# Optimization experiments

Measured on AMD Instinct MI355X. Metric: run time of the kernel, lower is better.

## Reference

```python
import jax, jax.numpy as jnp
import numpy as np

D_K = 64
EPS = 1e-6


def setup_inputs() -> dict:
    key = jax.random.key(0)
    ks = jax.random.split(key, 6)
    B, S, D2, DV = 4, 2048, 1024, 64
    q = jax.random.normal(ks[0], (B, S, D2), dtype=jnp.float32)
    k = jax.random.normal(ks[1], (B, S, D2), dtype=jnp.float32)
    v = jax.random.normal(ks[2], (B, S, D2), dtype=jnp.float32)
    mask = jax.random.randint(ks[3], (B, S, S), 0, 2) == 1
    V = jax.random.normal(ks[4], (1, DV), dtype=jnp.float32)
    fc_w = jax.random.normal(ks[5], (D2, DV), dtype=jnp.float32) * (1.0 / np.sqrt(DV))
    fc_b = jnp.zeros((D2,), dtype=jnp.float32)
    ln_g = jnp.ones((D2,), dtype=jnp.float32)
    ln_b = jnp.zeros((D2,), dtype=jnp.float32)
    return {"q": q, "k": k, "v": v, "mask": mask, "V": V,
            "fc_w": fc_w, "fc_b": fc_b, "ln_g": ln_g, "ln_b": ln_b}


def _layer_norm(x, g, b):
    mu = jnp.mean(x, axis=-1, keepdims=True)
    var = jnp.var(x, axis=-1, keepdims=True)
    return (x - mu) * jax.lax.rsqrt(var + EPS) * g + b


def reference(q, k, v, mask, V, fc_w, fc_b, ln_g, ln_b):
    residual = q
    qn = _layer_norm(q, ln_g, ln_b)
    # scaled dot-product scores (no softmax in this variant)
    attn = jnp.einsum('bsd,btd->bst', qn / jnp.sqrt(jnp.float32(D_K)), k)
    attn = jnp.where(mask, 0.0, attn)  # masked_fill with 0
    # v_ = V broadcast over (batch, seq, key); attn @ v_ == row-sum outer V
    output = jnp.sum(attn, axis=-1, keepdims=True) * V  # [B,S,d_v]
    output = output @ fc_w.T + fc_b                     # [B,S,2*d_model]
    output = output + residual
    return (output, attn)
```

## Files before the change

kernel.cpp:

```cpp
#include <hip/hip_runtime.h>
#include <hip/hip_bf16.h>
#include <cstdint>

#define S_LEN 2048
#define D2_   1024
#define DV_   64
#define NB_   4

typedef __bf16 bf16x8 __attribute__((ext_vector_type(8)));
typedef float  f32x4  __attribute__((ext_vector_type(4)));
typedef int    i32x4  __attribute__((ext_vector_type(4)));

__device__ __forceinline__ unsigned short f2bf(float f) {
  union { float f; unsigned int u; } v; v.f = f;
  unsigned int r = v.u + 0x7fffu + ((v.u >> 16) & 1u);
  return (unsigned short)(r >> 16);
}

__device__ __forceinline__ void async16(const unsigned short* g, unsigned short* l) {
  __builtin_amdgcn_global_load_lds(
      (__attribute__((address_space(1))) void*)g,
      (__attribute__((address_space(3))) void*)l,
      16, 0, 0);
}

__global__ void __launch_bounds__(256) prep_kernel(
    const float* __restrict__ q, const float* __restrict__ k,
    const float* __restrict__ gam, const float* __restrict__ bet,
    const float* __restrict__ V, const float* __restrict__ fw,
    unsigned short* __restrict__ qn, unsigned short* __restrict__ kb,
    float* __restrict__ w2, float* __restrict__ rowsum) {
  const int row = blockIdx.x;
  const int t = threadIdx.x;

  if (row < 32) rowsum[row * 256 + t] = 0.0f;

  const float4 x = ((const float4*)(q + (size_t)row * D2_))[t];
  float s  = x.x + x.y + x.z + x.w;
  float ss = x.x * x.x + x.y * x.y + x.z * x.z + x.w * x.w;
  #pragma unroll
  for (int o = 32; o > 0; o >>= 1) { s += __shfl_down(s, o); ss += __shfl_down(ss, o); }
  __shared__ float red[8];
  if ((t & 63) == 0) { red[t >> 6] = s; red[(t >> 6) + 4] = ss; }
  __syncthreads();
  const float tot  = red[0] + red[1] + red[2] + red[3];
  const float tots = red[4] + red[5] + red[6] + red[7];
  const float mu  = tot * (1.0f / D2_);
  const float var = tots * (1.0f / D2_) - mu * mu;
  const float rs  = rsqrtf(var + 1e-6f) * 0.125f;
  const float4 gv = ((const float4*)gam)[t];
  const float4 bv = ((const float4*)bet)[t];
  ushort4 o4;
  o4.x = f2bf((x.x - mu) * rs * gv.x + 0.125f * bv.x);
  o4.y = f2bf((x.y - mu) * rs * gv.y + 0.125f * bv.y);
  o4.z = f2bf((x.z - mu) * rs * gv.z + 0.125f * bv.z);
  o4.w = f2bf((x.w - mu) * rs * gv.w + 0.125f * bv.w);
  ((ushort4*)(qn + (size_t)row * D2_))[t] = o4;

  const float4 kx = ((const float4*)(k + (size_t)row * D2_))[t];
  ushort4 k4;
  k4.x = f2bf(kx.x); k4.y = f2bf(kx.y); k4.z = f2bf(kx.z); k4.w = f2bf(kx.w);
  ((ushort4*)(kb + (size_t)row * D2_))[t] = k4;

  if (row < 4) {
    const int d = row * 256 + t;
    const float4* r  = (const float4*)(fw + (size_t)d * DV_);
    const float4* vv = (const float4*)V;
    float acc = 0.f;
    #pragma unroll
    for (int j = 0; j < 16; ++j) {
      const float4 a = r[j], b = vv[j];
      acc += a.x * b.x + a.y * b.y + a.z * b.z + a.w * b.w;
    }
    w2[d] = acc;
  }
}

__global__ void __launch_bounds__(256, 2) attn_gemm_kernel(
    const unsigned short* __restrict__ qn,
    const unsigned short* __restrict__ kb,
    const int* __restrict__ mask,
    float* __restrict__ attn,
    float* __restrict__ rowsum) {
  __shared__ __align__(16) unsigned short Asm_[2 * 8192];
  __shared__ __align__(16) unsigned short Bsm_[2 * 8192];

  const int t = threadIdx.x;

  const int orig = blockIdx.x + 16 * (blockIdx.y + 16 * blockIdx.z);
  const int swz  = (orig & 7) * 128 + (orig >> 3);
  const int bn = (swz & 15) * 128;
  const int bm = ((swz >> 4) & 15) * 128;
  const int bt = swz >> 8;

  const int srow_ = t >> 3;
  const int pg_   = (t & 7) ^ (srow_ & 7);
  const unsigned short* gA = qn + ((size_t)bt * S_LEN + bm + srow_) * D2_ + pg_ * 8;
  const unsigned short* gB = kb + ((size_t)bt * S_LEN + bn + srow_) * D2_ + pg_ * 8;
  unsigned short* lA = Asm_ + t * 8;
  unsigned short* lB = Bsm_ + t * 8;

  const int lane = t & 63;
  const int w  = t >> 6;
  const int wm = (w >> 1) * 64;
  const int wn = (w & 1) * 64;
  const int lr = lane & 15;
  const int lg = lane >> 4;

  #define STAGE(buf, koff) do {                                     \
      _Pragma("unroll")                                             \
      for (int qq = 0; qq < 4; ++qq) {                              \
        async16(gA + (koff) + (size_t)qq * 32 * D2_, lA + (buf) + qq * 2048); \
        async16(gB + (koff) + (size_t)qq * 32 * D2_, lB + (buf) + qq * 2048); \
      }                                                             \
    } while (0)

  f32x4 acc[4][4] = {};

  auto compute = [&](int pl) {
    #pragma unroll
    for (int ks = 0; ks < 2; ++ks) {
      const int sl = ((ks << 2) + lg) ^ (lr & 7);
      bf16x8 af[4], bfv[4];
      #pragma unroll
      for (int f = 0; f < 4; ++f)
        af[f]  = *(const bf16x8*)(Asm_ + pl + (wm + f * 16 + lr) * 64 + sl * 8);
      #pragma unroll
      for (int f = 0; f < 4; ++f)
        bfv[f] = *(const bf16x8*)(Bsm_ + pl + (wn + f * 16 + lr) * 64 + sl * 8);
      #pragma unroll
      for (int fm = 0; fm < 4; ++fm)
        #pragma unroll
        for (int fn = 0; fn < 4; ++fn)
          acc[fm][fn] = __builtin_amdgcn_mfma_f32_16x16x32_bf16(
              bfv[fn], af[fm], acc[fm][fn], 0, 0, 0);
    }
  };

  STAGE(0, 0);
  STAGE(8192, 64);

  #pragma unroll 1
  for (int kt = 0; kt < 15; ++kt) {
    const int cur = (kt & 1) * 8192;
    asm volatile("s_waitcnt vmcnt(8)" ::: "memory");
    __builtin_amdgcn_s_barrier();
    compute(cur);
    __builtin_amdgcn_s_barrier();
    if (kt < 14) STAGE(cur, (kt + 2) * 64);
  }
  asm volatile("s_waitcnt vmcnt(0)" ::: "memory");
  __builtin_amdgcn_s_barrier();
  compute(8192);

  const int m_base = bm + wm + lr;
  const size_t rb0 = ((size_t)bt * S_LEN) * S_LEN;
  #pragma unroll
  for (int fm = 0; fm < 4; ++fm) {
    const int m = m_base + fm * 16;
    const size_t rowbase = rb0 + (size_t)m * S_LEN;
    float s = 0.f;
    #pragma unroll
    for (int fn = 0; fn < 4; ++fn) {
      const int n0 = bn + wn + fn * 16 + lg * 4;
      const i32x4 mk = __builtin_nontemporal_load((const i32x4*)(mask + rowbase + n0));
      f32x4 v;
      v[0] = mk[0] ? 0.0f : acc[fm][fn][0];
      v[1] = mk[1] ? 0.0f : acc[fm][fn][1];
      v[2] = mk[2] ? 0.0f : acc[fm][fn][2];
      v[3] = mk[3] ? 0.0f : acc[fm][fn][3];
      *(f32x4*)(attn + rowbase + n0) = v;
      s += v[0] + v[1] + v[2] + v[3];
    }
    s += __shfl_xor(s, 16);
    s += __shfl_xor(s, 32);
    if (lane < 16) atomicAdd(rowsum + (size_t)bt * S_LEN + m, s);
  }
  #undef STAGE
}

__global__ void __launch_bounds__(256) out_kernel(
    const float* __restrict__ rowsum, const float* __restrict__ q,
    const float* __restrict__ w2, const float* __restrict__ fcb,
    float* __restrict__ out) {
  const int row = blockIdx.x;
  const int t = threadIdx.x;
  const float rs = rowsum[row];
  const float4 wv = ((const float4*)w2)[t];
  const float4 bv = ((const float4*)fcb)[t];
  const float4 qv = ((const float4*)(q + (size_t)row * D2_))[t];
  float4 o4;
  o4.x = rs * wv.x + bv.x + qv.x;
  o4.y = rs * wv.y + bv.y + qv.y;
  o4.z = rs * wv.z + bv.z + qv.z;
  o4.w = rs * wv.w + bv.w + qv.w;
  ((float4*)(out + (size_t)row * D2_))[t] = o4;
}

extern "C" void kernel_launch(void* const* d_in, const int* in_sizes, int n_in,
                              void* d_out, int out_size, void* d_ws, size_t ws_size,
                              hipStream_t stream) {
  (void)in_sizes; (void)n_in; (void)out_size; (void)ws_size;
  const float* q    = (const float*)d_in[0];
  const float* k    = (const float*)d_in[1];
  const int*   mask = (const int*)d_in[3];
  const float* V    = (const float*)d_in[4];
  const float* fw   = (const float*)d_in[5];
  const float* fcb  = (const float*)d_in[6];
  const float* lg   = (const float*)d_in[7];
  const float* lb   = (const float*)d_in[8];

  float* out  = (float*)d_out;
  float* attn = out + (size_t)NB_ * S_LEN * D2_;

  unsigned short* qn = (unsigned short*)out;
  unsigned short* kb = qn + (size_t)NB_ * S_LEN * D2_;
  float* w2     = (float*)d_ws;
  float* rowsum = w2 + D2_;

  prep_kernel<<<NB_ * S_LEN, 256, 0, stream>>>(q, k, lg, lb, V, fw, qn, kb, w2, rowsum);
  attn_gemm_kernel<<<dim3(S_LEN / 128, S_LEN / 128, NB_), 256, 0, stream>>>(qn, kb, mask, attn, rowsum);
  out_kernel<<<NB_ * S_LEN, 256, 0, stream>>>(rowsum, q, w2, fcb, out);
}
```

Baseline: 269.8 us.

## Use 256x256 GEMM tiles with 512 threads and interleaved async staging

The attention GEMM goes from 128x128 tiles with 256 threads to 256x256 tiles with 512 threads (8 waves, each owning a 128x64 sub-tile). This raises operand reuse from LDS and halves global traffic per output. The next K-tile's async global-to-LDS loads are now split into small chunks issued between MFMA groups, and s_setprio is raised around the MFMA bursts. The cost is a larger accumulator footprint and more LDS (64KB), which limits occupancy. There are also only 256 blocks, so wave quantization on the CUs becomes a risk.

```diff
diff --git a/kernel.cpp b/kernel.cpp
--- a/kernel.cpp
+++ b/kernel.cpp
@@ -76,22 +76,22 @@
   }
 }
 
-__global__ void __launch_bounds__(256, 2) attn_gemm_kernel(
+__global__ void __launch_bounds__(512, 2) attn_gemm_kernel(
     const unsigned short* __restrict__ qn,
     const unsigned short* __restrict__ kb,
     const int* __restrict__ mask,
     float* __restrict__ attn,
     float* __restrict__ rowsum) {
-  __shared__ __align__(16) unsigned short Asm_[2 * 8192];
-  __shared__ __align__(16) unsigned short Bsm_[2 * 8192];
+  __shared__ __align__(16) unsigned short Asm_[2 * 16384];
+  __shared__ __align__(16) unsigned short Bsm_[2 * 16384];
 
   const int t = threadIdx.x;
 
-  const int orig = blockIdx.x + 16 * (blockIdx.y + 16 * blockIdx.z);
-  const int swz  = (orig & 7) * 128 + (orig >> 3);
-  const int bn = (swz & 15) * 128;
-  const int bm = ((swz >> 4) & 15) * 128;
-  const int bt = swz >> 8;
+  const int orig = blockIdx.x + 8 * (blockIdx.y + 8 * blockIdx.z);
+  const int swz  = (orig & 7) * 32 + (orig >> 3);
+  const int bn = (swz & 7) * 256;
+  const int bm = ((swz >> 3) & 7) * 256;
+  const int bt = swz >> 6;
 
   const int srow_ = t >> 3;
   const int pg_   = (t & 7) ^ (srow_ & 7);
@@ -102,61 +102,76 @@
 
   const int lane = t & 63;
   const int w  = t >> 6;
-  const int wm = (w >> 1) * 64;
-  const int wn = (w & 1) * 64;
+  const int wm = (w >> 2) * 128;
+  const int wn = (w & 3) * 64;
   const int lr = lane & 15;
   const int lg = lane >> 4;
 
-  #define STAGE(buf, koff) do {                                     \
-      _Pragma("unroll")                                             \
-      for (int qq = 0; qq < 4; ++qq) {                              \
-        async16(gA + (koff) + (size_t)qq * 32 * D2_, lA + (buf) + qq * 2048); \
-        async16(gB + (koff) + (size_t)qq * 32 * D2_, lB + (buf) + qq * 2048); \
-      }                                                             \
-    } while (0)
-
-  f32x4 acc[4][4] = {};
-
-  auto compute = [&](int pl) {
+  auto stage2 = [&](int dstbuf, int dtile, int mat, int s0) {
+    const unsigned short* g = mat ? gB : gA;
+    unsigned short* l = mat ? lB : lA;
+    #pragma unroll
+    for (int s = s0; s < s0 + 2; ++s)
+      async16(g + (size_t)dtile * 64 + (size_t)s * 64 * D2_, l + dstbuf + s * 4096);
+  };
+
+  f32x4 acc[8][4] = {};
+
+  auto group = [&](int src, int dst, int dtile, bool do_stage) {
     #pragma unroll
     for (int ks = 0; ks < 2; ++ks) {
       const int sl = ((ks << 2) + lg) ^ (lr & 7);
-      bf16x8 af[4], bfv[4];
+      bf16x8 bfv[4];
       #pragma unroll
-      for (int f = 0; f < 4; ++f)
-        af[f]  = *(const bf16x8*)(Asm_ + pl + (wm + f * 16 + lr) * 64 + sl * 8);
-      #pragma unroll
-      for (int f = 0; f < 4; ++f)
-        bfv[f] = *(const bf16x8*)(Bsm_ + pl + (wn + f * 16 + lr) * 64 + sl * 8);
-      #pragma unroll
-      for (int fm = 0; fm < 4; ++fm)
+      for (int mg = 0; mg < 2; ++mg) {
+        const int ph = ks * 2 + mg;
+        if (do_stage) stage2(dst, dtile, ph >> 1, (ph & 1) * 2);
+        if (mg == 0) {
+          #pragma unroll
+          for (int f = 0; f < 4; ++f)
+            bfv[f] = *(const bf16x8*)(Bsm_ + src + (wn + f * 16 + lr) * 64 + sl * 8);
+        }
+        bf16x8 af[4];
         #pragma unroll
-        for (int fn = 0; fn < 4; ++fn)
-          acc[fm][fn] = __builtin_amdgcn_mfma_f32_16x16x32_bf16(
-              bfv[fn], af[fm], acc[fm][fn], 0, 0, 0);
+        for (int f = 0; f < 4; ++f)
+          af[f] = *(const bf16x8*)(Asm_ + src + (wm + (mg * 4 + f) * 16 + lr) * 64 + sl * 8);
+        __builtin_amdgcn_s_setprio(1);
+        #pragma unroll
+        for (int f = 0; f < 4; ++f)
+          #pragma unroll
+          for (int fn = 0; fn < 4; ++fn)
+            acc[mg * 4 + f][fn] = __builtin_amdgcn_mfma_f32_16x16x32_bf16(
+                bfv[fn], af[f], acc[mg * 4 + f][fn], 0, 0, 0);
+        __builtin_amdgcn_s_setprio(0);
+      }
     }
   };
 
-  STAGE(0, 0);
-  STAGE(8192, 64);
-
-  #pragma unroll 1
-  for (int kt = 0; kt < 15; ++kt) {
-    const int cur = (kt & 1) * 8192;
-    asm volatile("s_waitcnt vmcnt(8)" ::: "memory");
-    __builtin_amdgcn_s_barrier();
-    compute(cur);
-    __builtin_amdgcn_s_barrier();
-    if (kt < 14) STAGE(cur, (kt + 2) * 64);
+  #pragma unroll
+  for (int s = 0; s < 4; ++s) {
+    async16(gA + (size_t)s * 64 * D2_, lA + s * 4096);
+    async16(gB + (size_t)s * 64 * D2_, lB + s * 4096);
   }
   asm volatile("s_waitcnt vmcnt(0)" ::: "memory");
   __builtin_amdgcn_s_barrier();
-  compute(8192);
+  asm volatile("" ::: "memory");
+
+  #pragma unroll 1
+  for (int kt = 0; kt < 16; kt += 2) {
+    group(0, 16384, kt + 1, true);
+    asm volatile("s_waitcnt vmcnt(0)" ::: "memory");
+    __builtin_amdgcn_s_barrier();
+    asm volatile("" ::: "memory");
+    group(16384, 0, kt + 2, kt + 2 < 16);
+    asm volatile("s_waitcnt vmcnt(0)" ::: "memory");
+    __builtin_amdgcn_s_barrier();
+    asm volatile("" ::: "memory");
+  }
 
   const int m_base = bm + wm + lr;
   const size_t rb0 = ((size_t)bt * S_LEN) * S_LEN;
   #pragma unroll
-  for (int fm = 0; fm < 4; ++fm) {
+  for (int fm = 0; fm < 8; ++fm) {
     const int m = m_base + fm * 16;
     const size_t rowbase = rb0 + (size_t)m * S_LEN;
     float s = 0.f;
@@ -176,7 +191,6 @@
     s += __shfl_xor(s, 32);
     if (lane < 16) atomicAdd(rowsum + (size_t)bt * S_LEN + m, s);
   }
-  #undef STAGE
 }
 
 __global__ void __launch_bounds__(256) out_kernel(
@@ -219,6 +233,6 @@
   float* rowsum = w2 + D2_;
 
   prep_kernel<<<NB_ * S_LEN, 256, 0, stream>>>(q, k, lg, lb, V, fw, qn, kb, w2, rowsum);
-  attn_gemm_kernel<<<dim3(S_LEN / 128, S_LEN / 128, NB_), 256, 0, stream>>>(qn, kb, mask, attn, rowsum);
+  attn_gemm_kernel<<<dim3(S_LEN / 256, S_LEN / 256, NB_), 512, 0, stream>>>(qn, kb, mask, attn, rowsum);
   out_kernel<<<NB_ * S_LEN, 256, 0, stream>>>(rowsum, q, w2, fcb, out);
 }
```

Result: no change. 266.3 us (-1.3%).
